# Optimization experiments

Hardware: AMD Instinct MI355X
Metric: run time of the kernel (lower is better)

Reference implementation:

```python
import jax, jax.numpy as jnp
import numpy as np

B, S, D, H = 2, 2048, 768, 12
DEPTH = D // H


def setup_inputs() -> dict:
    key = jax.random.key(0)
    ks = jax.random.split(key, 8)
    scale = 1.0 / np.sqrt(D)
    inp = {
        "query": jax.random.normal(ks[0], (B, S, D), jnp.float32),
        "key": jax.random.normal(ks[1], (B, S, D), jnp.float32),
        "value": jax.random.normal(ks[2], (B, S, D), jnp.float32),
        # additive mask convention: 1.0 where attention is disallowed (causal)
        "mask": jnp.triu(jnp.ones((1, 1, S, S), jnp.float32), k=1),
        "Wq": jax.random.normal(ks[3], (D, D), jnp.float32) * scale,
        "bq": jnp.zeros((D,), jnp.float32),
        "Wk": jax.random.normal(ks[4], (D, D), jnp.float32) * scale,
        "bk": jnp.zeros((D,), jnp.float32),
        "Wv": jax.random.normal(ks[5], (D, D), jnp.float32) * scale,
        "bv": jnp.zeros((D,), jnp.float32),
        "Wo": jax.random.normal(ks[6], (D, D), jnp.float32) * scale,
        "bo": jnp.zeros((D,), jnp.float32),
    }
    return inp


def _split_heads(x):
    # [B, S, D] -> [B, H, S, depth]
    b, s, _ = x.shape
    return x.reshape(b, s, H, DEPTH).transpose(0, 2, 1, 3)


def reference(query, key, value, mask, Wq, bq, Wk, bk, Wv, bv, Wo, bo):
    q = _split_heads(query @ Wq + bq)   # [B,H,S,depth]
    k = _split_heads(key @ Wk + bk)
    v = _split_heads(value @ Wv + bv)

    d_k = jnp.asarray(DEPTH, q.dtype)
    logits = jnp.einsum("bhqd,bhkd->bhqk", q, k) / jnp.sqrt(d_k)
    logits = logits + mask * -1e9
    weights = jax.nn.softmax(logits, axis=-1)          # [B,H,S,S] -- O(N^2)
    attn = jnp.einsum("bhqk,bhkd->bhqd", weights, v)    # [B,H,S,depth]

    concat = attn.transpose(0, 2, 1, 3).reshape(query.shape[0], -1, D)
    return concat @ Wo + bo
```

## Files before the change

### kernel.cpp

```cpp
#include <hip/hip_runtime.h>


typedef __bf16 bf16;
typedef __bf16 bf16x8 __attribute__((ext_vector_type(8)));
typedef __bf16 bf16x4 __attribute__((ext_vector_type(4)));
typedef float  f32x4  __attribute__((ext_vector_type(4)));

__device__ __forceinline__ void async_load16(const void* g, void* l) {
  __builtin_amdgcn_global_load_lds(
      (__attribute__((address_space(1))) void*)g,
      (__attribute__((address_space(3))) void*)l, 16, 0, 0);
}

__device__ __forceinline__ float rsum16(float x) {
#pragma unroll
  for (int m = 1; m < 16; m <<= 1) x += __shfl_xor(x, m, 16);
  return x;
}

__global__ __launch_bounds__(256) void convert_kernel(
    const float* __restrict__ q, const float* __restrict__ k,
    const float* __restrict__ v, bf16* __restrict__ qo,
    bf16* __restrict__ ko, bf16* __restrict__ vo) {
  const float* src; bf16* dst;
  if (blockIdx.y == 0)      { src = q; dst = qo; }
  else if (blockIdx.y == 1) { src = k; dst = ko; }
  else                      { src = v; dst = vo; }
  size_t i = ((size_t)blockIdx.x * 256 + threadIdx.x) * 8;
  f32x4 a = *(const f32x4*)(src + i);
  f32x4 b = *(const f32x4*)(src + i + 4);
  bf16x8 o;
  o[0]=(bf16)a[0]; o[1]=(bf16)a[1]; o[2]=(bf16)a[2]; o[3]=(bf16)a[3];
  o[4]=(bf16)b[0]; o[5]=(bf16)b[1]; o[6]=(bf16)b[2]; o[7]=(bf16)b[3];
  *(bf16x8*)(dst + i) = o;
}

__global__ __launch_bounds__(256) void transpose_w_kernel(
    const float* __restrict__ W0, const float* __restrict__ W1,
    const float* __restrict__ W2, const float* __restrict__ W3,
    bf16* __restrict__ T0, bf16* __restrict__ T1,
    bf16* __restrict__ T2, bf16* __restrict__ T3) {
  const float* W; bf16* T;
  switch (blockIdx.z) {
    case 0: W = W0; T = T0; break;
    case 1: W = W1; T = T1; break;
    case 2: W = W2; T = T2; break;
    default: W = W3; T = T3; break;
  }
  __shared__ float tile[32][33];
  const int tx = threadIdx.x, ty = threadIdx.y;
  const int k0 = blockIdx.y * 32, n0 = blockIdx.x * 32;
#pragma unroll
  for (int j = 0; j < 32; j += 8)
    tile[ty + j][tx] = W[(size_t)(k0 + ty + j) * 768 + n0 + tx];
  __syncthreads();
#pragma unroll
  for (int j = 0; j < 32; j += 8) {
    int n = ty + j;
    T[(size_t)(n0 + n) * 768 + k0 + tx] = (bf16)tile[tx][n];
  }
}

__device__ __forceinline__ void gemm_body(
    const bf16* __restrict__ A, const bf16* __restrict__ Wt,
    const float* __restrict__ bias, void* __restrict__ outp,
    int m0, int n0, int mode, char* smem) {
  const int t = threadIdx.x;
  const int w = t >> 6, lane = t & 63;
  const int wm = w >> 1, wn = w & 1;
  const int quad = lane >> 4, l15 = lane & 15;
  const int srow = lane >> 3, k8p = lane & 7;

  size_t offA[4], offB[4];
  int ldsOff[4];
#pragma unroll
  for (int i = 0; i < 4; ++i) {
    const int rl = w * 32 + i * 8 + srow;
    const int kk = k8p ^ (rl & 7);
    offA[i] = (size_t)(m0 + rl) * 768 + kk * 8;
    offB[i] = (size_t)(n0 + rl) * 768 + kk * 8;
    ldsOff[i] = (w * 32 + i * 8) * 64;
  }

  f32x4 acc[4][4] = {};

#pragma unroll
  for (int i = 0; i < 4; ++i) {
    async_load16(A  + offA[i], smem + 2 * ldsOff[i]);
    async_load16(Wt + offB[i], smem + 16384 + 2 * ldsOff[i]);
  }

  for (int kidx = 0; kidx < 12; ++kidx) {
    __syncthreads();
    if (kidx < 11) {
      const int nb = (kidx + 1) & 1;
      const int k1 = (kidx + 1) * 64;
#pragma unroll
      for (int i = 0; i < 4; ++i) {
        async_load16(A  + offA[i] + k1, smem + nb * 32768 + 2 * ldsOff[i]);
        async_load16(Wt + offB[i] + k1, smem + nb * 32768 + 16384 + 2 * ldsOff[i]);
      }
    }
    const bf16* As = (const bf16*)(smem + (kidx & 1) * 32768);
    const bf16* Bs = (const bf16*)(smem + (kidx & 1) * 32768 + 16384);
#pragma unroll
    for (int ks = 0; ks < 2; ++ks) {
      bf16x8 af[4], bfv[4];
      const int slot = (((ks * 4 + quad) ^ (lane & 7)) * 8);
#pragma unroll
      for (int mi = 0; mi < 4; ++mi)
        af[mi] = *(const bf16x8*)(As + (wm * 64 + mi * 16 + l15) * 64 + slot);
#pragma unroll
      for (int ni = 0; ni < 4; ++ni)
        bfv[ni] = *(const bf16x8*)(Bs + (wn * 64 + ni * 16 + l15) * 64 + slot);
#pragma unroll
      for (int mi = 0; mi < 4; ++mi)
#pragma unroll
        for (int ni = 0; ni < 4; ++ni)
          acc[mi][ni] = __builtin_amdgcn_mfma_f32_16x16x32_bf16(af[mi], bfv[ni], acc[mi][ni], 0, 0, 0);
    }
  }

#pragma unroll
  for (int ni = 0; ni < 4; ++ni) {
    const float bc = bias[n0 + wn * 64 + ni * 16 + l15];
#pragma unroll
    for (int mi = 0; mi < 4; ++mi)
#pragma unroll
      for (int r = 0; r < 4; ++r) acc[mi][ni][r] += bc;
  }

  if (mode == 2) {
    float* outf = (float*)outp;
#pragma unroll
    for (int ni = 0; ni < 4; ++ni) {
      const int col = n0 + wn * 64 + ni * 16 + l15;
#pragma unroll
      for (int mi = 0; mi < 4; ++mi) {
        const int row = m0 + wm * 64 + mi * 16 + quad * 4;
#pragma unroll
        for (int r = 0; r < 4; ++r)
          outf[(size_t)(row + r) * 768 + col] = acc[mi][ni][r];
      }
    }
    return;
  }

  __syncthreads();
  bf16* outb = (bf16*)outp;
  if (mode == 0) {
    bf16* Ce = (bf16*)smem;
#pragma unroll
    for (int ni = 0; ni < 4; ++ni) {
      const int col = wn * 64 + ni * 16 + l15;
#pragma unroll
      for (int mi = 0; mi < 4; ++mi) {
        const int row = wm * 64 + mi * 16 + quad * 4;
#pragma unroll
        for (int r = 0; r < 4; ++r)
          Ce[(row + r) * 136 + col] = (bf16)acc[mi][ni][r];
      }
    }
    __syncthreads();
#pragma unroll
    for (int j = 0; j < 8; ++j) {
      const int ci = j * 256 + t;
      const int row = ci >> 4, c8 = (ci & 15) * 8;
      bf16x8 vv = *(const bf16x8*)(Ce + row * 136 + c8);
      const int rg = m0 + row, cg = n0 + c8;
      const int bb = rg >> 11, s = rg & 2047;
      const int h = cg >> 6, d = cg & 63;
      *(bf16x8*)(outb + ((size_t)(bb * 12 + h) * 2048 + s) * 64 + d) = vv;
    }
  } else {
    bf16* Ct = (bf16*)smem;
#pragma unroll
    for (int ni = 0; ni < 4; ++ni) {
      const int col = wn * 64 + ni * 16 + l15;
#pragma unroll
      for (int mi = 0; mi < 4; ++mi) {
        const int row = wm * 64 + mi * 16 + quad * 4;
        bf16x4 pv;
        pv[0] = (bf16)acc[mi][ni][0]; pv[1] = (bf16)acc[mi][ni][1];
        pv[2] = (bf16)acc[mi][ni][2]; pv[3] = (bf16)acc[mi][ni][3];
        *(bf16x4*)(Ct + (size_t)col * 136 + row) = pv;
      }
    }
    __syncthreads();
#pragma unroll
    for (int j = 0; j < 8; ++j) {
      const int ci = j * 256 + t;
      const int col = ci >> 4, r8 = (ci & 15) * 8;
      bf16x8 vv = *(const bf16x8*)(Ct + col * 136 + r8);
      const int cg = n0 + col;
      const int h = cg >> 6, d = cg & 63;
      const int rg = m0 + r8;
      const int bb = rg >> 11, s = rg & 2047;
      *(bf16x8*)(outb + ((size_t)(bb * 12 + h) * 64 + d) * 2048 + s) = vv;
    }
  }
}

__global__ __launch_bounds__(256) void gemm_qkv_kernel(
    const bf16* __restrict__ A0, const bf16* __restrict__ A1, const bf16* __restrict__ A2,
    const bf16* __restrict__ W0, const bf16* __restrict__ W1, const bf16* __restrict__ W2,
    const float* __restrict__ b0, const float* __restrict__ b1, const float* __restrict__ b2,
    bf16* __restrict__ Q, bf16* __restrict__ K, bf16* __restrict__ V) {
  __shared__ __align__(16) char smem[65536];
  const int z = blockIdx.z;
  const bf16* A  = (z == 0) ? A0 : (z == 1) ? A1 : A2;
  const bf16* Wt = (z == 0) ? W0 : (z == 1) ? W1 : W2;
  const float* bias = (z == 0) ? b0 : (z == 1) ? b1 : b2;
  void* outp = (z == 0) ? (void*)Q : (z == 1) ? (void*)K : (void*)V;
  gemm_body(A, Wt, bias, outp, blockIdx.y * 128, blockIdx.x * 128, (z == 2) ? 1 : 0, smem);
}

__global__ __launch_bounds__(256) void gemm_out_kernel(
    const bf16* __restrict__ A, const bf16* __restrict__ Wt,
    const float* __restrict__ bias, float* __restrict__ out) {
  __shared__ __align__(16) char smem[65536];
  gemm_body(A, Wt, bias, (void*)out, blockIdx.y * 128, blockIdx.x * 128, 2, smem);
}

__global__ __launch_bounds__(256) void attn_kernel(
    const bf16* __restrict__ Qh, const bf16* __restrict__ Kh,
    const bf16* __restrict__ Vt, bf16* __restrict__ attnb) {
  __shared__ __align__(16) char smem[49152];
  bf16* Ps = (bf16*)(smem + 32768);

  const int t = threadIdx.x;
  const int w = t >> 6, lane = t & 63, quad = lane >> 4, l15 = lane & 15;
  const int srow = lane >> 3, k8p = lane & 7;
  const int qt = 15 - (int)blockIdx.x;
  const int bh = blockIdx.y;
  const int q0 = qt * 128;
  const bf16* Qp = Qh + (size_t)bh * (2048 * 64);
  const bf16* Kp = Kh + (size_t)bh * (2048 * 64);
  const bf16* Vp = Vt + (size_t)bh * (64 * 2048);

  size_t offK[2], offV[2];
  int ldsOff[2];
#pragma unroll
  for (int i = 0; i < 2; ++i) {
    const int rl = w * 16 + i * 8 + srow;
    const int kk = k8p ^ (rl & 7);
    offK[i] = (size_t)rl * 64 + kk * 8;
    offV[i] = (size_t)rl * 2048 + kk * 8;
    ldsOff[i] = (w * 16 + i * 8) * 64;
  }

  bf16x8 qf[2][2];
#pragma unroll
  for (int mi = 0; mi < 2; ++mi)
#pragma unroll
    for (int ks = 0; ks < 2; ++ks) {
      const int qrow = q0 + w * 32 + mi * 16 + l15;
      qf[mi][ks] = *(const bf16x8*)(Qp + (size_t)qrow * 64 + ks * 32 + quad * 8);
    }

  f32x4 o[2][4] = {};
  float lp[2][4] = {};

  const float sc = 0.125f * 1.44269504f;
  const int nkt = qt * 2 + 2;

#pragma unroll
  for (int i = 0; i < 2; ++i) {
    async_load16(Kp + offK[i], smem + 2 * ldsOff[i]);
    async_load16(Vp + offV[i], smem + 8192 + 2 * ldsOff[i]);
  }

  for (int kt = 0; kt < nkt; ++kt) {
    const int k0 = kt * 64;
    const int cur = kt & 1;
    __syncthreads();
    if (kt + 1 < nkt) {
      const int nb = cur ^ 1;
#pragma unroll
      for (int i = 0; i < 2; ++i) {
        async_load16(Kp + offK[i] + (size_t)(k0 + 64) * 64, smem + nb * 16384 + 2 * ldsOff[i]);
        async_load16(Vp + offV[i] + (k0 + 64),              smem + nb * 16384 + 8192 + 2 * ldsOff[i]);
      }
    }
    const bf16* Ks = (const bf16*)(smem + cur * 16384);
    const bf16* Vs = (const bf16*)(smem + cur * 16384 + 8192);

    f32x4 s[2][4] = {};
#pragma unroll
    for (int ks = 0; ks < 2; ++ks) {
      const int slot = (((ks * 4 + quad) ^ (lane & 7)) * 8);
      bf16x8 kf[4];
#pragma unroll
      for (int ni = 0; ni < 4; ++ni)
        kf[ni] = *(const bf16x8*)(Ks + (ni * 16 + l15) * 64 + slot);
#pragma unroll
      for (int mi = 0; mi < 2; ++mi)
#pragma unroll
        for (int ni = 0; ni < 4; ++ni)
          s[mi][ni] = __builtin_amdgcn_mfma_f32_16x16x32_bf16(qf[mi][ks], kf[ni], s[mi][ni], 0, 0, 0);
    }

    const bool diag = (k0 + 63 > q0);
#pragma unroll
    for (int mi = 0; mi < 2; ++mi)
#pragma unroll
      for (int ni = 0; ni < 4; ++ni) {
        const int key = ni * 16 + l15;
        const int perm = key >> 3;
#pragma unroll
        for (int r = 0; r < 4; ++r) {
          const int q = w * 32 + mi * 16 + quad * 4 + r;
          float p = __builtin_amdgcn_exp2f(s[mi][ni][r] * sc);
          if (diag && (k0 + key > q0 + q)) p = 0.0f;
          lp[mi][r] += p;
          Ps[q * 64 + ((perm ^ (q & 7)) * 8) + (key & 7)] = (bf16)p;
        }
      }

#pragma unroll
    for (int ks = 0; ks < 2; ++ks) {
      const int slot = (((ks * 4 + quad) ^ (lane & 7)) * 8);
      bf16x8 pf[2], vfr[4];
#pragma unroll
      for (int mi = 0; mi < 2; ++mi)
        pf[mi] = *(const bf16x8*)(Ps + (w * 32 + mi * 16 + l15) * 64 + slot);
#pragma unroll
      for (int di = 0; di < 4; ++di)
        vfr[di] = *(const bf16x8*)(Vs + (di * 16 + l15) * 64 + slot);
#pragma unroll
      for (int mi = 0; mi < 2; ++mi)
#pragma unroll
        for (int di = 0; di < 4; ++di)
          o[mi][di] = __builtin_amdgcn_mfma_f32_16x16x32_bf16(pf[mi], vfr[di], o[mi][di], 0, 0, 0);
    }
  }

  const int bb = bh / 12, h = bh % 12;
#pragma unroll
  for (int mi = 0; mi < 2; ++mi) {
    float inv[4];
#pragma unroll
    for (int r = 0; r < 4; ++r) inv[r] = 1.0f / rsum16(lp[mi][r]);
#pragma unroll
    for (int di = 0; di < 4; ++di) {
      const int col = h * 64 + di * 16 + l15;
#pragma unroll
      for (int r = 0; r < 4; ++r) {
        const int row = bb * 2048 + q0 + w * 32 + mi * 16 + quad * 4 + r;
        attnb[(size_t)row * 768 + col] = (bf16)(o[mi][di][r] * inv[r]);
      }
    }
  }
}

extern "C" void kernel_launch(void* const* d_in, const int* in_sizes, int n_in,
                              void* d_out, int out_size, void* d_ws, size_t ws_size,
                              hipStream_t stream) {
  const float* query = (const float*)d_in[0];
  const float* key   = (const float*)d_in[1];
  const float* value = (const float*)d_in[2];
  const float* Wq = (const float*)d_in[4];
  const float* bq = (const float*)d_in[5];
  const float* Wk = (const float*)d_in[6];
  const float* bk = (const float*)d_in[7];
  const float* Wv = (const float*)d_in[8];
  const float* bv = (const float*)d_in[9];
  const float* Wo = (const float*)d_in[10];
  const float* bo = (const float*)d_in[11];
  float* out = (float*)d_out;

  char* ws = (char*)d_ws;
  constexpr size_t SZ_X = (size_t)4096 * 768 * 2;
  constexpr size_t SZ_W = (size_t)768 * 768 * 2;
  bf16* qb   = (bf16*)(ws);
  bf16* kb   = (bf16*)(ws + SZ_X);
  bf16* vb   = (bf16*)(ws + 2 * SZ_X);
  bf16* wtq  = (bf16*)(ws + 3 * SZ_X);
  bf16* wtk  = (bf16*)(ws + 3 * SZ_X + SZ_W);
  bf16* wtv  = (bf16*)(ws + 3 * SZ_X + 2 * SZ_W);
  bf16* wto  = (bf16*)(ws + 3 * SZ_X + 3 * SZ_W);
  bf16* Qh   = (bf16*)(ws + 3 * SZ_X + 4 * SZ_W);
  bf16* Kh   = (bf16*)(ws + 4 * SZ_X + 4 * SZ_W);
  bf16* Vtb  = (bf16*)(ws + 5 * SZ_X + 4 * SZ_W);
  bf16* attb = (bf16*)(ws + 6 * SZ_X + 4 * SZ_W);

  convert_kernel<<<dim3(1536, 3), 256, 0, stream>>>(query, key, value, qb, kb, vb);
  transpose_w_kernel<<<dim3(24, 24, 4), dim3(32, 8), 0, stream>>>(Wq, Wk, Wv, Wo, wtq, wtk, wtv, wto);
  gemm_qkv_kernel<<<dim3(6, 32, 3), 256, 0, stream>>>(qb, kb, vb, wtq, wtk, wtv, bq, bk, bv, Qh, Kh, Vtb);
  attn_kernel<<<dim3(16, 24), 256, 0, stream>>>(Qh, Kh, Vtb, attb);
  gemm_out_kernel<<<dim3(6, 32), 256, 0, stream>>>(attb, wto, bo, out);
}
```

Measured before the change: 219.6 us.

## Split long causal attention rows across two blocks and merge partials

Query tiles in the upper half of the sequence have their key range split at tile 16 across a second grid z-slice. Each slice writes unnormalised fp32 partial outputs and row sums, and a new combine kernel adds the partials, normalises and writes the bf16 concat buffer. This evens out the causal load imbalance, where the last query tiles did twice the key tiles of the middle ones. The QK^T MFMA is also transposed so each lane owns a query row, which lets P be stored as packed bf16x4 and row sums be reduced with two shuffles. The cost is an extra launch and fp32 partial traffic, written into workspace regions (old bf16 inputs and wtq) that are dead by this point.

```diff
diff --git a/kernel.cpp b/kernel.cpp
--- a/kernel.cpp
+++ b/kernel.cpp
@@ -10,12 +10,6 @@
   __builtin_amdgcn_global_load_lds(
       (__attribute__((address_space(1))) void*)g,
       (__attribute__((address_space(3))) void*)l, 16, 0, 0);
-}
-
-__device__ __forceinline__ float rsum16(float x) {
-#pragma unroll
-  for (int m = 1; m < 16; m <<= 1) x += __shfl_xor(x, m, 16);
-  return x;
 }
 
 __global__ __launch_bounds__(256) void convert_kernel(
@@ -224,19 +218,27 @@
 
 __global__ __launch_bounds__(256) void attn_kernel(
     const bf16* __restrict__ Qh, const bf16* __restrict__ Kh,
-    const bf16* __restrict__ Vt, bf16* __restrict__ attnb) {
+    const bf16* __restrict__ Vt, float* __restrict__ O0, float* __restrict__ O1,
+    float* __restrict__ L0, float* __restrict__ L1) {
+  const int qt = 15 - (int)blockIdx.x;
+  const int z = blockIdx.z;
+  if (z == 1 && qt < 8) return;
+
   __shared__ __align__(16) char smem[49152];
   bf16* Ps = (bf16*)(smem + 32768);
 
   const int t = threadIdx.x;
   const int w = t >> 6, lane = t & 63, quad = lane >> 4, l15 = lane & 15;
   const int srow = lane >> 3, k8p = lane & 7;
-  const int qt = 15 - (int)blockIdx.x;
   const int bh = blockIdx.y;
   const int q0 = qt * 128;
   const bf16* Qp = Qh + (size_t)bh * (2048 * 64);
   const bf16* Kp = Kh + (size_t)bh * (2048 * 64);
   const bf16* Vp = Vt + (size_t)bh * (64 * 2048);
+
+  const int ntiles = 2 * qt + 2;
+  const int kt_begin = z ? 16 : 0;
+  const int kt_end = z ? ntiles : (ntiles < 16 ? ntiles : 16);
 
   size_t offK[2], offV[2];
   int ldsOff[2];
@@ -259,22 +261,21 @@
     }
 
   f32x4 o[2][4] = {};
-  float lp[2][4] = {};
+  float lp[2] = {0.f, 0.f};
 
   const float sc = 0.125f * 1.44269504f;
-  const int nkt = qt * 2 + 2;
 
 #pragma unroll
   for (int i = 0; i < 2; ++i) {
-    async_load16(Kp + offK[i], smem + 2 * ldsOff[i]);
-    async_load16(Vp + offV[i], smem + 8192 + 2 * ldsOff[i]);
-  }
-
-  for (int kt = 0; kt < nkt; ++kt) {
+    async_load16(Kp + offK[i] + (size_t)kt_begin * 64 * 64, smem + 2 * ldsOff[i]);
+    async_load16(Vp + offV[i] + (size_t)kt_begin * 64,      smem + 8192 + 2 * ldsOff[i]);
+  }
+
+  for (int kt = kt_begin; kt < kt_end; ++kt) {
     const int k0 = kt * 64;
     const int cur = kt & 1;
     __syncthreads();
-    if (kt + 1 < nkt) {
+    if (kt + 1 < kt_end) {
       const int nb = cur ^ 1;
 #pragma unroll
       for (int i = 0; i < 2; ++i) {
@@ -285,7 +286,7 @@
     const bf16* Ks = (const bf16*)(smem + cur * 16384);
     const bf16* Vs = (const bf16*)(smem + cur * 16384 + 8192);
 
-    f32x4 s[2][4] = {};
+    f32x4 st[4][2] = {};
 #pragma unroll
     for (int ks = 0; ks < 2; ++ks) {
       const int slot = (((ks * 4 + quad) ^ (lane & 7)) * 8);
@@ -294,28 +295,31 @@
       for (int ni = 0; ni < 4; ++ni)
         kf[ni] = *(const bf16x8*)(Ks + (ni * 16 + l15) * 64 + slot);
 #pragma unroll
-      for (int mi = 0; mi < 2; ++mi)
-#pragma unroll
-        for (int ni = 0; ni < 4; ++ni)
-          s[mi][ni] = __builtin_amdgcn_mfma_f32_16x16x32_bf16(qf[mi][ks], kf[ni], s[mi][ni], 0, 0, 0);
+      for (int ni = 0; ni < 4; ++ni)
+#pragma unroll
+        for (int mi = 0; mi < 2; ++mi)
+          st[ni][mi] = __builtin_amdgcn_mfma_f32_16x16x32_bf16(kf[ni], qf[mi][ks], st[ni][mi], 0, 0, 0);
     }
 
     const bool diag = (k0 + 63 > q0);
 #pragma unroll
-    for (int mi = 0; mi < 2; ++mi)
+    for (int mi = 0; mi < 2; ++mi) {
+      const int q_local = w * 32 + mi * 16 + l15;
+      const int qg = q0 + q_local;
 #pragma unroll
       for (int ni = 0; ni < 4; ++ni) {
-        const int key = ni * 16 + l15;
-        const int perm = key >> 3;
+        bf16x4 pv;
 #pragma unroll
         for (int r = 0; r < 4; ++r) {
-          const int q = w * 32 + mi * 16 + quad * 4 + r;
-          float p = __builtin_amdgcn_exp2f(s[mi][ni][r] * sc);
-          if (diag && (k0 + key > q0 + q)) p = 0.0f;
-          lp[mi][r] += p;
-          Ps[q * 64 + ((perm ^ (q & 7)) * 8) + (key & 7)] = (bf16)p;
+          float p = __builtin_amdgcn_exp2f(st[ni][mi][r] * sc);
+          if (diag && (k0 + ni * 16 + quad * 4 + r > qg)) p = 0.0f;
+          lp[mi] += p;
+          pv[r] = (bf16)p;
         }
-      }
+        const int c = ni * 2 + (quad >> 1);
+        *(bf16x4*)(Ps + q_local * 64 + ((c ^ (q_local & 7)) << 3) + ((quad & 1) << 2)) = pv;
+      }
+    }
 
 #pragma unroll
     for (int ks = 0; ks < 2; ++ks) {
@@ -335,22 +339,51 @@
     }
   }
 
-  const int bb = bh / 12, h = bh % 12;
+  float* Op; float* Lp_;
+  size_t rbase;
+  if (z == 0) { Op = O0; Lp_ = L0; rbase = (size_t)bh * 2048 + q0; }
+  else        { Op = O1; Lp_ = L1; rbase = (size_t)bh * 1024 + (qt - 8) * 128; }
+
 #pragma unroll
   for (int mi = 0; mi < 2; ++mi) {
-    float inv[4];
-#pragma unroll
-    for (int r = 0; r < 4; ++r) inv[r] = 1.0f / rsum16(lp[mi][r]);
+    float l = lp[mi];
+    l += __shfl_xor(l, 16);
+    l += __shfl_xor(l, 32);
+    if (quad == 0) Lp_[rbase + w * 32 + mi * 16 + l15] = l;
 #pragma unroll
     for (int di = 0; di < 4; ++di) {
-      const int col = h * 64 + di * 16 + l15;
+      const int d = di * 16 + l15;
 #pragma unroll
       for (int r = 0; r < 4; ++r) {
-        const int row = bb * 2048 + q0 + w * 32 + mi * 16 + quad * 4 + r;
-        attnb[(size_t)row * 768 + col] = (bf16)(o[mi][di][r] * inv[r]);
-      }
-    }
-  }
+        const size_t row = rbase + w * 32 + mi * 16 + quad * 4 + r;
+        Op[row * 64 + d] = o[mi][di][r];
+      }
+    }
+  }
+}
+
+__global__ __launch_bounds__(256) void combine_kernel(
+    const float* __restrict__ O0, const float* __restrict__ O1,
+    const float* __restrict__ L0, const float* __restrict__ L1,
+    bf16* __restrict__ attb) {
+  const int idx = blockIdx.x * 256 + threadIdx.x;
+  const int row = idx >> 4;
+  const int dd = (idx & 15) << 2;
+  const int bh = row >> 11, s = row & 2047;
+  f32x4 o = *(const f32x4*)(O0 + (size_t)row * 64 + dd);
+  float l = L0[row];
+  if (s >= 1024) {
+    const size_t r1 = (size_t)bh * 1024 + (s - 1024);
+    f32x4 o1 = *(const f32x4*)(O1 + r1 * 64 + dd);
+    o[0] += o1[0]; o[1] += o1[1]; o[2] += o1[2]; o[3] += o1[3];
+    l += L1[r1];
+  }
+  const float inv = 1.0f / l;
+  bf16x4 ov;
+  ov[0] = (bf16)(o[0] * inv); ov[1] = (bf16)(o[1] * inv);
+  ov[2] = (bf16)(o[2] * inv); ov[3] = (bf16)(o[3] * inv);
+  const int b = bh / 12, h = bh % 12;
+  *(bf16x4*)(attb + ((size_t)(b * 2048 + s)) * 768 + h * 64 + dd) = ov;
 }
 
 extern "C" void kernel_launch(void* const* d_in, const int* in_sizes, int n_in,
@@ -383,10 +416,15 @@
   bf16* Kh   = (bf16*)(ws + 4 * SZ_X + 4 * SZ_W);
   bf16* Vtb  = (bf16*)(ws + 5 * SZ_X + 4 * SZ_W);
   bf16* attb = (bf16*)(ws + 6 * SZ_X + 4 * SZ_W);
+  float* O0 = (float*)(ws);
+  float* O1 = (float*)(ws + 2 * SZ_X);
+  float* L0 = (float*)(ws + 3 * SZ_X);
+  float* L1 = (float*)(ws + 3 * SZ_X + 196608);
 
   convert_kernel<<<dim3(1536, 3), 256, 0, stream>>>(query, key, value, qb, kb, vb);
   transpose_w_kernel<<<dim3(24, 24, 4), dim3(32, 8), 0, stream>>>(Wq, Wk, Wv, Wo, wtq, wtk, wtv, wto);
   gemm_qkv_kernel<<<dim3(6, 32, 3), 256, 0, stream>>>(qb, kb, vb, wtq, wtk, wtv, bq, bk, bv, Qh, Kh, Vtb);
-  attn_kernel<<<dim3(16, 24), 256, 0, stream>>>(Qh, Kh, Vtb, attb);
+  attn_kernel<<<dim3(16, 24, 2), 256, 0, stream>>>(Qh, Kh, Vtb, O0, O1, L0, L1);
+  combine_kernel<<<dim3(3072), 256, 0, stream>>>(O0, O1, L0, L1, attb);
   gemm_out_kernel<<<dim3(6, 32), 256, 0, stream>>>(attb, wto, bo, out);
 }
```

New measurement: 204.9 us. 1.07x faster.
